# Optimization experiments

Measured on AMD Instinct MI355X. Metric: run time of the kernel, lower is better.

The kernel has to match this reference:

```python
import jax, jax.numpy as jnp
import numpy as np

N_NODES = 100000
N_EDGES = 1600000
IN_CH = 128          # 127 node features + 1 node_attr
HIDDEN = 2           # hidd_FV_size
OUT_CH = 128
ATTR = 6


def setup_inputs() -> dict:
    key = jax.random.key(0)
    ks = jax.random.split(key, 8)
    x = jax.random.normal(ks[0], (N_NODES, IN_CH - 1), dtype=jnp.float32)
    node_attr = jax.random.normal(ks[1], (N_NODES, 1), dtype=jnp.float32)
    edge_index = jax.random.randint(ks[2], (2, N_EDGES), 0, N_NODES, dtype=jnp.int64)
    edge_attr = jax.random.normal(ks[3], (N_EDGES, ATTR), dtype=jnp.float32)
    # lin_in: Linear(ATTR, HIDDEN * IN_CH); lin_out: Linear(HIDDEN * IN_CH, OUT_CH)
    W_in = jax.random.normal(ks[4], (ATTR, HIDDEN * IN_CH), dtype=jnp.float32) / np.sqrt(ATTR)
    b_in = jax.random.normal(ks[5], (HIDDEN * IN_CH,), dtype=jnp.float32) * 0.01
    W_out = jax.random.normal(ks[6], (HIDDEN * IN_CH, OUT_CH), dtype=jnp.float32) / np.sqrt(HIDDEN * IN_CH)
    b_out = jax.random.normal(ks[7], (OUT_CH,), dtype=jnp.float32) * 0.01
    return {"x": x, "node_attr": node_attr, "edge_index": edge_index,
            "edge_attr": edge_attr, "W_in": W_in, "b_in": b_in,
            "W_out": W_out, "b_out": b_out}


def reference(x, node_attr, edge_index, edge_attr, W_in, b_in, W_out, b_out):
    # forward: x = cat(x, node_attr) -> propagate(aggr='add') -> update
    xc = jnp.concatenate([x, node_attr], axis=1)                # [N, IN_CH]
    src, dst = edge_index[0], edge_index[1]                     # PyG: message from x_j=src, aggregated at dst
    x_j = xc[src]                                               # [E, IN_CH] gather
    # message: scaling = relu(lin_in(edge_attr)); result = scaling.reshape(E,C,H) * x_j[...,None]
    scaling = jax.nn.relu(edge_attr @ W_in + b_in)              # [E, C*H]
    msg = (scaling.reshape(-1, IN_CH, HIDDEN) * x_j[:, :, None]).reshape(-1, IN_CH * HIDDEN)
    # aggregate: scatter-add over destination nodes
    aggr = jax.ops.segment_sum(msg, dst, num_segments=N_NODES)  # [N, C*H]
    # update: lin_out -> tanh (dropout p=0 / eval mode)
    return jnp.tanh(aggr @ W_out + b_out)                       # [N, OUT_CH]
```

## Files before the change

### kernel.cpp

```cpp
#include <hip/hip_runtime.h>


#define ATTR 6
#define SCAN_CHUNK 1024


__device__ __forceinline__ float2 f2fma(float2 a, float2 b, float2 c) {
  return make_float2(fmaf(a.x, b.x, c.x), fmaf(a.y, b.y, c.y));
}
__device__ __forceinline__ float2 f2splat(float x) { return make_float2(x, x); }


__global__ __launch_bounds__(256) void hist_kernel(
    const int* __restrict__ ei, int* __restrict__ counts, int E)
{
  const int e0 = blockIdx.x * 1024 + threadIdx.x * 4;
  if (((E & 3) == 0) && (e0 + 4 <= E)) {
    const int4 d = *(const int4*)(ei + E + e0);
    atomicAdd(&counts[d.x], 1);
    atomicAdd(&counts[d.y], 1);
    atomicAdd(&counts[d.z], 1);
    atomicAdd(&counts[d.w], 1);
  } else {
#pragma unroll
    for (int j = 0; j < 4; ++j) {
      const int e = e0 + j;
      if (e < E) atomicAdd(&counts[ei[E + e]], 1);
    }
  }
}


__global__ __launch_bounds__(256) void scan1_kernel(
    const int* __restrict__ counts, int* __restrict__ offsets,
    int* __restrict__ bsum, int N)
{
  __shared__ int sdata[256];
  const int t = threadIdx.x;
  const int base = blockIdx.x * SCAN_CHUNK + t * 4;
  int c[4]; int s = 0;
#pragma unroll
  for (int j = 0; j < 4; ++j) { int i = base + j; c[j] = (i < N) ? counts[i] : 0; s += c[j]; }
  sdata[t] = s;
  __syncthreads();
  for (int d = 1; d < 256; d <<= 1) {
    int tv = (t >= d) ? sdata[t - d] : 0;
    __syncthreads();
    sdata[t] += tv;
    __syncthreads();
  }
  int excl = sdata[t] - s;
#pragma unroll
  for (int j = 0; j < 4; ++j) { int i = base + j; if (i < N) offsets[i] = excl; excl += c[j]; }
  if (t == 255) bsum[blockIdx.x] = sdata[255];
}


__global__ __launch_bounds__(256) void scanB_kernel(
    int* __restrict__ offsets, int* __restrict__ cursors,
    const int* __restrict__ bsum, int N, int E)
{
  __shared__ int red[4];
  const int t = threadIdx.x;
  int v = 0;
  for (int k = t; k < (int)blockIdx.x; k += 256) v += bsum[k];
#pragma unroll
  for (int d = 32; d > 0; d >>= 1) v += __shfl_down(v, d, 64);
  if ((t & 63) == 0) red[t >> 6] = v;
  __syncthreads();
  const int add = red[0] + red[1] + red[2] + red[3];

  const int base = blockIdx.x * SCAN_CHUNK + t * 4;
#pragma unroll
  for (int j = 0; j < 4; ++j) {
    const int i = base + j;
    if (i < N) { const int o = offsets[i] + add; offsets[i] = o; cursors[i] = o; }
  }
  if (blockIdx.x == 0 && t == 0) offsets[N] = E;
}


__global__ __launch_bounds__(256) void scatter_concat2_kernel(
    const int* __restrict__ ei, const float* __restrict__ ea,
    int* __restrict__ cursors, float* __restrict__ pay,
    const float* __restrict__ x, const float* __restrict__ na,
    float* __restrict__ xc, int E, int N, int SB)
{
  if ((int)blockIdx.x < SB) {
    const int e = blockIdx.x * 256 + threadIdx.x;
    if (e < E) {
      const int dst = ei[E + e];
      const int slot = atomicAdd(&cursors[dst], 1);
      const float2 a0 = *(const float2*)(ea + e * ATTR + 0);
      const float2 a1 = *(const float2*)(ea + e * ATTR + 2);
      const float2 a2 = *(const float2*)(ea + e * ATTR + 4);
      float4* pp = (float4*)pay + 2 * slot;
      pp[0] = make_float4(__int_as_float(ei[e]), a0.x, a0.y, a1.x);
      pp[1] = make_float4(a1.y, a2.x, a2.y, 0.f);
    }
  } else {
    const int gid = (blockIdx.x - SB) * 256 + threadIdx.x;
    const int row = gid >> 5;
    const int c4 = (gid & 31) * 4;
    if (row < N) {
      const float* xr = x + row * 127;
      float4 v;
      v.x = xr[c4];
      v.y = xr[c4 + 1];
      v.z = xr[c4 + 2];
      v.w = (c4 == 124) ? na[row] : xr[c4 + 3];
      *(float4*)(xc + row * 128 + c4) = v;
    }
  }
}


#define EDGE_MATH4(P0, P1, XV)                                                \
  {                                                                           \
    const float e0f = (P0).y;                                                 \
    const float e1f = (P0).z;                                                 \
    const float e2f = (P0).w;                                                 \
    const float e3f = (P1).x;                                                 \
    const float e4f = (P1).y;                                                 \
    const float e5f = (P1).z;                                                 \
    float sa0 = bA.x, sa1 = bA.y, sb0 = bB.x, sb1 = bB.y;                     \
    sa0 = fmaf(e0f, wA[0].x, sa0); sa1 = fmaf(e0f, wA[0].y, sa1);             \
    sb0 = fmaf(e0f, wB[0].x, sb0); sb1 = fmaf(e0f, wB[0].y, sb1);             \
    sa0 = fmaf(e1f, wA[1].x, sa0); sa1 = fmaf(e1f, wA[1].y, sa1);             \
    sb0 = fmaf(e1f, wB[1].x, sb0); sb1 = fmaf(e1f, wB[1].y, sb1);             \
    sa0 = fmaf(e2f, wA[2].x, sa0); sa1 = fmaf(e2f, wA[2].y, sa1);             \
    sb0 = fmaf(e2f, wB[2].x, sb0); sb1 = fmaf(e2f, wB[2].y, sb1);             \
    sa0 = fmaf(e3f, wA[3].x, sa0); sa1 = fmaf(e3f, wA[3].y, sa1);             \
    sb0 = fmaf(e3f, wB[3].x, sb0); sb1 = fmaf(e3f, wB[3].y, sb1);             \
    sa0 = fmaf(e4f, wA[4].x, sa0); sa1 = fmaf(e4f, wA[4].y, sa1);             \
    sb0 = fmaf(e4f, wB[4].x, sb0); sb1 = fmaf(e4f, wB[4].y, sb1);             \
    sa0 = fmaf(e5f, wA[5].x, sa0); sa1 = fmaf(e5f, wA[5].y, sa1);             \
    sb0 = fmaf(e5f, wB[5].x, sb0); sb1 = fmaf(e5f, wB[5].y, sb1);             \
    sa0 = fmaxf(sa0, 0.f); sa1 = fmaxf(sa1, 0.f);                             \
    sb0 = fmaxf(sb0, 0.f); sb1 = fmaxf(sb1, 0.f);                             \
    accA.x = fmaf(sa0, (XV).x, accA.x); accA.y = fmaf(sa1, (XV).x, accA.y);   \
    accB.x = fmaf(sb0, (XV).y, accB.x); accB.y = fmaf(sb1, (XV).y, accB.y);   \
  }

__global__ __launch_bounds__(256) void aggregate_v7_kernel(
    const float* __restrict__ xc,
    const float* __restrict__ W_in, const float* __restrict__ b_in,
    const int* __restrict__ offsets, const float* __restrict__ pay,
    float* __restrict__ aggr, int N)
{
  const int L = (int)threadIdx.x & 63;
  const int n = __builtin_amdgcn_readfirstlane((int)blockIdx.x * 4 + ((int)threadIdx.x >> 6));
  if (n >= N) return;

  float2 wA[ATTR], wB[ATTR];
#pragma unroll
  for (int a = 0; a < ATTR; ++a) {
    const float4 w4 = *(const float4*)(W_in + a * 256 + 4 * L);
    wA[a] = make_float2(w4.x, w4.y);
    wB[a] = make_float2(w4.z, w4.w);
  }
  const float4 b4 = *(const float4*)(b_in + 4 * L);
  const float2 bA = make_float2(b4.x, b4.y);
  const float2 bB = make_float2(b4.z, b4.w);

  float2 accA = make_float2(0.f, 0.f);
  float2 accB = make_float2(0.f, 0.f);
  const int beg = __builtin_amdgcn_readfirstlane(offsets[n]);
  const int end = __builtin_amdgcn_readfirstlane(offsets[n + 1]);
  const int lane2 = 2 * L;
  const float4* pp = (const float4*)pay;

  int i = beg;
  const int nfull = (end - beg) >> 1;

  if (nfull > 0) {
    float4 c0a = pp[2 * (size_t)i + 0], c1a = pp[2 * (size_t)i + 1];
    float4 c0b = pp[2 * (size_t)i + 2], c1b = pp[2 * (size_t)i + 3];
    float2 ga = *(const float2*)(xc + (unsigned)__float_as_int(c0a.x) * 128u + lane2);
    float2 gb = *(const float2*)(xc + (unsigned)__float_as_int(c0b.x) * 128u + lane2);
    const int i1 = (nfull > 1) ? i + 2 : i;
    float4 n0a = pp[2 * (size_t)i1 + 0], n1a = pp[2 * (size_t)i1 + 1];
    float4 n0b = pp[2 * (size_t)i1 + 2], n1b = pp[2 * (size_t)i1 + 3];

#pragma unroll 2
    for (int g = 0; g < nfull; ++g, i += 2) {
      float2 ha = *(const float2*)(xc + (unsigned)__float_as_int(n0a.x) * 128u + lane2);
      float2 hb = *(const float2*)(xc + (unsigned)__float_as_int(n0b.x) * 128u + lane2);
      const int ip = (g + 2 < nfull) ? i + 4 : i;
      float4 f0a = pp[2 * (size_t)ip + 0], f1a = pp[2 * (size_t)ip + 1];
      float4 f0b = pp[2 * (size_t)ip + 2], f1b = pp[2 * (size_t)ip + 3];

      EDGE_MATH4(c0a, c1a, ga);
      EDGE_MATH4(c0b, c1b, gb);

      c0a = n0a; c1a = n1a; c0b = n0b; c1b = n1b;
      n0a = f0a; n1a = f1a; n0b = f0b; n1b = f1b;
      ga = ha; gb = hb;
    }
  }

  if (i < end) {
    const float4 p0 = pp[2 * (size_t)i + 0];
    const float4 p1 = pp[2 * (size_t)i + 1];
    const float2 xv = *(const float2*)(xc + (unsigned)__float_as_int(p0.x) * 128u + lane2);
    EDGE_MATH4(p0, p1, xv);
  }

  *(float4*)(aggr + n * 256 + 4 * L) = make_float4(accA.x, accA.y, accB.x, accB.y);
}


__global__ __launch_bounds__(256) void scatter_concat_kernel(
    const int* __restrict__ ei, const float* __restrict__ ea,
    int* __restrict__ cursors, int* __restrict__ srcs, float* __restrict__ eas,
    const float* __restrict__ x, const float* __restrict__ na,
    float* __restrict__ xc, int E, int N, int SB)
{
  if ((int)blockIdx.x < SB) {
    const int e = blockIdx.x * 256 + threadIdx.x;
    if (e < E) {
      const int dst = ei[E + e];
      const int slot = atomicAdd(&cursors[dst], 1);
      srcs[slot] = ei[e];
      const float2 a0 = *(const float2*)(ea + (size_t)e * ATTR + 0);
      const float2 a1 = *(const float2*)(ea + (size_t)e * ATTR + 2);
      const float2 a2 = *(const float2*)(ea + (size_t)e * ATTR + 4);
      float* ep = eas + (size_t)slot * ATTR;
      *(float2*)(ep + 0) = a0;
      *(float2*)(ep + 2) = a1;
      *(float2*)(ep + 4) = a2;
    }
  } else {
    const int gid = (blockIdx.x - SB) * 256 + threadIdx.x;
    const int row = gid >> 5;
    const int c4 = (gid & 31) * 4;
    if (row < N) {
      const float* xr = x + (size_t)row * 127;
      float4 v;
      v.x = xr[c4];
      v.y = xr[c4 + 1];
      v.z = xr[c4 + 2];
      v.w = (c4 == 124) ? na[row] : xr[c4 + 3];
      *(float4*)(xc + (size_t)row * 128 + c4) = v;
    }
  }
}

__global__ __launch_bounds__(256) void aggregate8b_kernel(
    const float* __restrict__ xc,
    const float* __restrict__ W_in, const float* __restrict__ b_in,
    const int* __restrict__ offsets, const int* __restrict__ srcs,
    const float* __restrict__ eas,
    float* __restrict__ aggr, int N)
{
  const int L = threadIdx.x & 63;
  const int n = __builtin_amdgcn_readfirstlane(blockIdx.x * 4 + (threadIdx.x >> 6));
  if (n >= N) return;

  float2 wlo[ATTR], whi[ATTR];
#pragma unroll
  for (int a = 0; a < ATTR; ++a) {
    wlo[a] = *(const float2*)(W_in + a * 256 + 2 * L);
    whi[a] = *(const float2*)(W_in + a * 256 + 128 + 2 * L);
  }
  const float2 blo = *(const float2*)(b_in + 2 * L);
  const float2 bhi = *(const float2*)(b_in + 128 + 2 * L);

  float alo0 = 0.f, alo1 = 0.f, ahi0 = 0.f, ahi1 = 0.f;
  const int beg = __builtin_amdgcn_readfirstlane(offsets[n]);
  const int end = __builtin_amdgcn_readfirstlane(offsets[n + 1]);

  for (int i0 = beg; i0 < end; ++i0) {
    const int s = srcs[i0];
    float eav[ATTR];
#pragma unroll
    for (int a = 0; a < ATTR; ++a) eav[a] = eas[(size_t)i0 * ATTR + a];
    const float* xr = xc + (size_t)s * 128;
    const float xl = xr[L];
    const float xh = xr[64 + L];
    float sl0 = blo.x, sl1 = blo.y, sh0 = bhi.x, sh1 = bhi.y;
#pragma unroll
    for (int a = 0; a < ATTR; ++a) {
      sl0 = fmaf(eav[a], wlo[a].x, sl0);
      sl1 = fmaf(eav[a], wlo[a].y, sl1);
      sh0 = fmaf(eav[a], whi[a].x, sh0);
      sh1 = fmaf(eav[a], whi[a].y, sh1);
    }
    sl0 = fmaxf(sl0, 0.f); sl1 = fmaxf(sl1, 0.f);
    sh0 = fmaxf(sh0, 0.f); sh1 = fmaxf(sh1, 0.f);
    alo0 = fmaf(sl0, xl, alo0);
    alo1 = fmaf(sl1, xl, alo1);
    ahi0 = fmaf(sh0, xh, ahi0);
    ahi1 = fmaf(sh1, xh, ahi1);
  }

  *(float2*)(aggr + (size_t)n * 256 + 2 * L)       = make_float2(alo0, alo1);
  *(float2*)(aggr + (size_t)n * 256 + 128 + 2 * L) = make_float2(ahi0, ahi1);
}


__global__ __launch_bounds__(256) void scatter_kernel(
    const int* __restrict__ ei, int* __restrict__ cursors,
    int* __restrict__ perm, int* __restrict__ srcs, int E)
{
  int e = blockIdx.x * 256 + threadIdx.x;
  if (e < E) {
    int dst = ei[E + e];
    int slot = atomicAdd(&cursors[dst], 1);
    perm[slot] = e;
    srcs[slot] = ei[e];
  }
}

__global__ __launch_bounds__(256) void aggregate4_kernel(
    const float* __restrict__ x, const float* __restrict__ node_attr,
    const int* __restrict__ ei, const float* __restrict__ ea,
    const float* __restrict__ W_in, const float* __restrict__ b_in,
    const int* __restrict__ offsets, const int* __restrict__ perm,
    const int* __restrict__ srcs,
    float* __restrict__ aggr, int N)
{
  const int L = threadIdx.x & 63;
  const int n = __builtin_amdgcn_readfirstlane(blockIdx.x * 4 + (threadIdx.x >> 6));
  if (n >= N) return;

  float2 wlo[ATTR], whi[ATTR];
#pragma unroll
  for (int a = 0; a < ATTR; ++a) {
    wlo[a] = *(const float2*)(W_in + a * 256 + 2 * L);
    whi[a] = *(const float2*)(W_in + a * 256 + 128 + 2 * L);
  }
  const float2 blo = *(const float2*)(b_in + 2 * L);
  const float2 bhi = *(const float2*)(b_in + 128 + 2 * L);

  float alo0 = 0.f, alo1 = 0.f, ahi0 = 0.f, ahi1 = 0.f;
  const int beg = offsets[n], end = offsets[n + 1];

  for (int i0 = beg; i0 < end; i0 += 4) {
    const int cnt = end - i0;
    int e4[4], s4[4];
#pragma unroll
    for (int j = 0; j < 4; ++j) {
      const int idx = i0 + ((j < cnt) ? j : cnt - 1);
      e4[j] = perm[idx];
      s4[j] = srcs[idx];
    }
    float eav[4][ATTR];
#pragma unroll
    for (int j = 0; j < 4; ++j)
#pragma unroll
      for (int a = 0; a < ATTR; ++a) eav[j][a] = ea[(size_t)e4[j] * ATTR + a];
    float xlo[4], xhi[4];
#pragma unroll
    for (int j = 0; j < 4; ++j) {
      const float* xr = x + (size_t)s4[j] * 127;
      xlo[j] = xr[L];
      xhi[j] = (L == 63) ? node_attr[s4[j]] : xr[64 + L];
    }
#pragma unroll
    for (int j = 0; j < 4; ++j)
      if (j >= cnt) { xlo[j] = 0.f; xhi[j] = 0.f; }
#pragma unroll
    for (int j = 0; j < 4; ++j) {
      float sl0 = blo.x, sl1 = blo.y, sh0 = bhi.x, sh1 = bhi.y;
#pragma unroll
      for (int a = 0; a < ATTR; ++a) {
        sl0 = fmaf(eav[j][a], wlo[a].x, sl0);
        sl1 = fmaf(eav[j][a], wlo[a].y, sl1);
        sh0 = fmaf(eav[j][a], whi[a].x, sh0);
        sh1 = fmaf(eav[j][a], whi[a].y, sh1);
      }
      sl0 = fmaxf(sl0, 0.f); sl1 = fmaxf(sl1, 0.f);
      sh0 = fmaxf(sh0, 0.f); sh1 = fmaxf(sh1, 0.f);
      alo0 = fmaf(sl0, xlo[j], alo0);
      alo1 = fmaf(sl1, xlo[j], alo1);
      ahi0 = fmaf(sh0, xhi[j], ahi0);
      ahi1 = fmaf(sh1, xhi[j], ahi1);
    }
  }

  *(float2*)(aggr + (size_t)n * 256 + 2 * L)       = make_float2(alo0, alo1);
  *(float2*)(aggr + (size_t)n * 256 + 128 + 2 * L) = make_float2(ahi0, ahi1);
}


__global__ __launch_bounds__(256) void edge_kernel(
    const float* __restrict__ x, const float* __restrict__ node_attr,
    const int* __restrict__ ei, const float* __restrict__ ea,
    const float* __restrict__ W_in, const float* __restrict__ b_in,
    float* __restrict__ aggr, int E, int N, int epw)
{
  const int lane = threadIdx.x & 63;
  const int wave = blockIdx.x * (blockDim.x >> 6) + (threadIdx.x >> 6);
  const int k0 = lane << 2;
  const int c0 = lane << 1;

  float w[ATTR][4];
#pragma unroll
  for (int a = 0; a < ATTR; ++a) {
    const float4 t = *(const float4*)(W_in + a * 256 + k0);
    w[a][0] = t.x; w[a][1] = t.y; w[a][2] = t.z; w[a][3] = t.w;
  }
  const float4 bt = *(const float4*)(b_in + k0);

  const long e0 = (long)wave * epw;
  for (int i = 0; i < epw; ++i) {
    const long e = e0 + i;
    if (e >= E) return;
    const int src = ei[e];
    const int dst = ei[E + e];

    float eav[ATTR];
#pragma unroll
    for (int a = 0; a < ATTR; ++a) eav[a] = ea[(size_t)e * ATTR + a];

    float s0 = bt.x, s1 = bt.y, s2 = bt.z, s3 = bt.w;
#pragma unroll
    for (int a = 0; a < ATTR; ++a) {
      s0 = fmaf(eav[a], w[a][0], s0);
      s1 = fmaf(eav[a], w[a][1], s1);
      s2 = fmaf(eav[a], w[a][2], s2);
      s3 = fmaf(eav[a], w[a][3], s3);
    }
    s0 = fmaxf(s0, 0.f); s1 = fmaxf(s1, 0.f);
    s2 = fmaxf(s2, 0.f); s3 = fmaxf(s3, 0.f);

    const float* xr = x + (size_t)src * 127;
    const float x0 = xr[c0];
    const float x1 = (lane == 63) ? node_attr[src] : xr[c0 + 1];

    float* ap = aggr + (size_t)dst * 256 + k0;
    atomicAdd(ap + 0, s0 * x0);
    atomicAdd(ap + 1, s1 * x0);
    atomicAdd(ap + 2, s2 * x1);
    atomicAdd(ap + 3, s3 * x1);
  }
}


__global__ __launch_bounds__(256) void node_kernel3(
    const float* __restrict__ aggr, const float* __restrict__ W_out,
    const float* __restrict__ b_out, float* __restrict__ out, int N)
{
  __shared__ float Wl[64 * 128];
  __shared__ float Al[64][68];
  const int t = threadIdx.x;
  const int o4 = (t & 31) * 4;
  const int ng = t >> 5;
  const int nbase = blockIdx.x * 64;

  float2 acc[8][2];
#pragma unroll
  for (int j = 0; j < 8; ++j) {
    acc[j][0] = make_float2(0.f, 0.f);
    acc[j][1] = make_float2(0.f, 0.f);
  }

  for (int kc = 0; kc < 4; ++kc) {
    __syncthreads();
    const float4* wsrc = (const float4*)(W_out + kc * 64 * 128);
    float4* wdst = (float4*)Wl;
#pragma unroll
    for (int i = 0; i < 8; ++i) wdst[t + 256 * i] = wsrc[t + 256 * i];
    {
      const int r = t >> 2, q = t & 3;
      int row = nbase + r; if (row >= N) row = N - 1;
      const float4* asrc = (const float4*)(aggr + (size_t)row * 256 + kc * 64 + q * 16);
      float4 v0 = asrc[0], v1 = asrc[1], v2 = asrc[2], v3 = asrc[3];
      float4* adst = (float4*)&Al[r][q * 16];
      adst[0] = v0; adst[1] = v1; adst[2] = v2; adst[3] = v3;
    }
    __syncthreads();

    for (int k = 0; k < 64; k += 4) {
      float4 a4[8];
#pragma unroll
      for (int j = 0; j < 8; ++j) a4[j] = *(const float4*)&Al[ng * 8 + j][k];
#pragma unroll
      for (int kk = 0; kk < 4; ++kk) {
        const float4 w4 = *(const float4*)&Wl[(k + kk) * 128 + o4];
        const float2 wA = make_float2(w4.x, w4.y);
        const float2 wB = make_float2(w4.z, w4.w);
#pragma unroll
        for (int j = 0; j < 8; ++j) {
          const float2 av = f2splat((&a4[j].x)[kk]);
          acc[j][0] = f2fma(av, wA, acc[j][0]);
          acc[j][1] = f2fma(av, wB, acc[j][1]);
        }
      }
    }
  }

  const float4 b4 = *(const float4*)(b_out + o4);
#pragma unroll
  for (int j = 0; j < 8; ++j) {
    const int n = nbase + ng * 8 + j;
    if (n < N) {
      float4 r;
      r.x = tanhf(acc[j][0].x + b4.x);
      r.y = tanhf(acc[j][0].y + b4.y);
      r.z = tanhf(acc[j][1].x + b4.z);
      r.w = tanhf(acc[j][1].y + b4.w);
      *(float4*)(out + (size_t)n * 128 + o4) = r;
    }
  }
}


extern "C" void kernel_launch(void* const* d_in, const int* in_sizes, int n_in,
                              void* d_out, int out_size, void* d_ws, size_t ws_size,
                              hipStream_t stream) {
  const float* x         = (const float*)d_in[0];
  const float* node_attr = (const float*)d_in[1];
  const int*   ei        = (const int*)d_in[2];
  const float* ea        = (const float*)d_in[3];
  const float* W_in      = (const float*)d_in[4];
  const float* b_in      = (const float*)d_in[5];
  const float* W_out     = (const float*)d_in[6];
  const float* b_out     = (const float*)d_in[7];
  float* out = (float*)d_out;

  const int N = in_sizes[0] / 127;
  const int E = in_sizes[2] / 2;

  auto align16 = [](size_t v) { return (v + 15) & ~(size_t)15; };
  const size_t szCounts  = align16((size_t)N * 4);
  const size_t szOffsets = align16(((size_t)N + 1) * 4);
  const size_t szCursors = align16((size_t)N * 4);
  const size_t szBsum    = align16(((size_t)N / SCAN_CHUNK + 2) * 4);
  const size_t szPerm    = align16((size_t)E * 4);
  const size_t szSrcs    = align16((size_t)E * 4);
  const size_t szEas     = align16((size_t)E * ATTR * 4);
  const size_t szPay     = align16((size_t)E * 8 * 4);
  const size_t szXc      = align16((size_t)N * 128 * 4);
  const size_t szAggr    = (size_t)N * 256 * 4;

  const size_t needA2 = szCounts + szOffsets + szCursors + szBsum +
                        szPay + szXc + szAggr;
  const size_t needA  = szCounts + szOffsets + szCursors + szBsum +
                        szSrcs + szEas + szXc + szAggr;
  const size_t needB  = szCounts + szOffsets + szCursors + szBsum +
                        szPerm + szSrcs + szAggr;

  const int nodeBlocks = (N + 63) / 64;
  const int histBlocks = (E + 1023) / 1024;
  const int nb = (N + SCAN_CHUNK - 1) / SCAN_CHUNK;
  const int SB = (E + 255) / 256;
  const int CB = (N * 32 + 255) / 256;

  if (ws_size >= needA2) {
    char* p = (char*)d_ws;
    int* counts   = (int*)p;     p += szCounts;
    int* offsets  = (int*)p;     p += szOffsets;
    int* cursors  = (int*)p;     p += szCursors;
    int* bsum     = (int*)p;     p += szBsum;
    float* pay    = (float*)p;   p += szPay;
    float* xc     = (float*)p;   p += szXc;
    float* aggr   = (float*)p;

    hipMemsetAsync(counts, 0, szCounts, stream);
    hist_kernel<<<histBlocks, 256, 0, stream>>>(ei, counts, E);
    scan1_kernel<<<nb, 256, 0, stream>>>(counts, offsets, bsum, N);
    scanB_kernel<<<nb, 256, 0, stream>>>(offsets, cursors, bsum, N, E);
    scatter_concat2_kernel<<<SB + CB, 256, 0, stream>>>(
        ei, ea, cursors, pay, x, node_attr, xc, E, N, SB);
    aggregate_v7_kernel<<<(N + 3) / 4, 256, 0, stream>>>(
        xc, W_in, b_in, offsets, pay, aggr, N);
    node_kernel3<<<nodeBlocks, 256, 0, stream>>>(aggr, W_out, b_out, out, N);
  } else if (ws_size >= needA) {
    char* p = (char*)d_ws;
    int* counts   = (int*)p;     p += szCounts;
    int* offsets  = (int*)p;     p += szOffsets;
    int* cursors  = (int*)p;     p += szCursors;
    int* bsum     = (int*)p;     p += szBsum;
    int* srcs     = (int*)p;     p += szSrcs;
    float* eas    = (float*)p;   p += szEas;
    float* xc     = (float*)p;   p += szXc;
    float* aggr   = (float*)p;

    hipMemsetAsync(counts, 0, szCounts, stream);
    hist_kernel<<<histBlocks, 256, 0, stream>>>(ei, counts, E);
    scan1_kernel<<<nb, 256, 0, stream>>>(counts, offsets, bsum, N);
    scanB_kernel<<<nb, 256, 0, stream>>>(offsets, cursors, bsum, N, E);
    scatter_concat_kernel<<<SB + CB, 256, 0, stream>>>(
        ei, ea, cursors, srcs, eas, x, node_attr, xc, E, N, SB);
    aggregate8b_kernel<<<(N + 3) / 4, 256, 0, stream>>>(
        xc, W_in, b_in, offsets, srcs, eas, aggr, N);
    node_kernel3<<<nodeBlocks, 256, 0, stream>>>(aggr, W_out, b_out, out, N);
  } else if (ws_size >= needB) {
    char* p = (char*)d_ws;
    int* counts   = (int*)p;     p += szCounts;
    int* offsets  = (int*)p;     p += szOffsets;
    int* cursors  = (int*)p;     p += szCursors;
    int* bsum     = (int*)p;     p += szBsum;
    int* perm     = (int*)p;     p += szPerm;
    int* srcs     = (int*)p;     p += szSrcs;
    float* aggr   = (float*)p;

    hipMemsetAsync(counts, 0, szCounts, stream);
    hist_kernel<<<histBlocks, 256, 0, stream>>>(ei, counts, E);
    scan1_kernel<<<nb, 256, 0, stream>>>(counts, offsets, bsum, N);
    scanB_kernel<<<nb, 256, 0, stream>>>(offsets, cursors, bsum, N, E);
    scatter_kernel<<<SB, 256, 0, stream>>>(ei, cursors, perm, srcs, E);
    aggregate4_kernel<<<(N + 3) / 4, 256, 0, stream>>>(
        x, node_attr, ei, ea, W_in, b_in, offsets, perm, srcs, aggr, N);
    node_kernel3<<<nodeBlocks, 256, 0, stream>>>(aggr, W_out, b_out, out, N);
  } else {
    float* aggr = (float*)d_ws;
    hipMemsetAsync(aggr, 0, (size_t)N * 256 * 4, stream);
    const int EPW = 4;
    const int waves = (E + EPW - 1) / EPW;
    edge_kernel<<<(waves + 3) / 4, 256, 0, stream>>>(
        x, node_attr, ei, ea, W_in, b_in, aggr, E, N, EPW);
    node_kernel3<<<nodeBlocks, 256, 0, stream>>>(aggr, W_out, b_out, out, N);
  }
}
```

Baseline: 536.9 us.

## Record per-edge rank during histogram to drop cursor atomics in scatter

The histogram kernel now stores each edge's atomicAdd return value as a 16-bit rank, so the scatter pass computes its slot as offsets[dst]+rank with no second round of atomics on cursors. The xc concatenation moves into the histogram launch, and the scan no longer writes a cursor array. In exchange it writes and reads an extra E*2-byte rank buffer, and it assumes in-degree fits in 16 bits. Edge order within a segment stays nondeterministic.

```diff
diff --git a/kernel.cpp b/kernel.cpp
--- a/kernel.cpp
+++ b/kernel.cpp
@@ -9,6 +9,46 @@
   return make_float2(fmaf(a.x, b.x, c.x), fmaf(a.y, b.y, c.y));
 }
 __device__ __forceinline__ float2 f2splat(float x) { return make_float2(x, x); }
+
+
+__global__ __launch_bounds__(256) void hist_rank_concat_kernel(
+    const int* __restrict__ ei, int* __restrict__ counts,
+    unsigned short* __restrict__ rank,
+    const float* __restrict__ x, const float* __restrict__ na,
+    float* __restrict__ xc, int E, int N, int SBH)
+{
+  if ((int)blockIdx.x < SBH) {
+    const int e0 = blockIdx.x * 1024 + threadIdx.x * 4;
+    if (((E & 3) == 0) && (e0 + 4 <= E)) {
+      const int4 d = *(const int4*)(ei + E + e0);
+      ushort4 r;
+      r.x = (unsigned short)atomicAdd(&counts[d.x], 1);
+      r.y = (unsigned short)atomicAdd(&counts[d.y], 1);
+      r.z = (unsigned short)atomicAdd(&counts[d.z], 1);
+      r.w = (unsigned short)atomicAdd(&counts[d.w], 1);
+      *(ushort4*)(rank + e0) = r;
+    } else {
+#pragma unroll
+      for (int j = 0; j < 4; ++j) {
+        const int e = e0 + j;
+        if (e < E) rank[e] = (unsigned short)atomicAdd(&counts[ei[E + e]], 1);
+      }
+    }
+  } else {
+    const int gid = (blockIdx.x - SBH) * 256 + threadIdx.x;
+    const int row = gid >> 5;
+    const int c4 = (gid & 31) * 4;
+    if (row < N) {
+      const float* xr = x + row * 127;
+      float4 v;
+      v.x = xr[c4];
+      v.y = xr[c4 + 1];
+      v.z = xr[c4 + 2];
+      v.w = (c4 == 124) ? na[row] : xr[c4 + 3];
+      *(float4*)(xc + row * 128 + c4) = v;
+    }
+  }
+}
 
 
 __global__ __launch_bounds__(256) void hist_kernel(
@@ -56,9 +96,8 @@
 }
 
 
-__global__ __launch_bounds__(256) void scanB_kernel(
-    int* __restrict__ offsets, int* __restrict__ cursors,
-    const int* __restrict__ bsum, int N, int E)
+__global__ __launch_bounds__(256) void scanB2_kernel(
+    int* __restrict__ offsets, const int* __restrict__ bsum, int N, int E)
 {
   __shared__ int red[4];
   const int t = threadIdx.x;
@@ -74,9 +113,52 @@
 #pragma unroll
   for (int j = 0; j < 4; ++j) {
     const int i = base + j;
+    if (i < N) offsets[i] += add;
+  }
+  if (blockIdx.x == 0 && t == 0) offsets[N] = E;
+}
+
+
+__global__ __launch_bounds__(256) void scanB_kernel(
+    int* __restrict__ offsets, int* __restrict__ cursors,
+    const int* __restrict__ bsum, int N, int E)
+{
+  __shared__ int red[4];
+  const int t = threadIdx.x;
+  int v = 0;
+  for (int k = t; k < (int)blockIdx.x; k += 256) v += bsum[k];
+#pragma unroll
+  for (int d = 32; d > 0; d >>= 1) v += __shfl_down(v, d, 64);
+  if ((t & 63) == 0) red[t >> 6] = v;
+  __syncthreads();
+  const int add = red[0] + red[1] + red[2] + red[3];
+
+  const int base = blockIdx.x * SCAN_CHUNK + t * 4;
+#pragma unroll
+  for (int j = 0; j < 4; ++j) {
+    const int i = base + j;
     if (i < N) { const int o = offsets[i] + add; offsets[i] = o; cursors[i] = o; }
   }
   if (blockIdx.x == 0 && t == 0) offsets[N] = E;
+}
+
+
+__global__ __launch_bounds__(256) void scatter_pay_kernel(
+    const int* __restrict__ ei, const unsigned short* __restrict__ rank,
+    const int* __restrict__ offsets, const float* __restrict__ ea,
+    float* __restrict__ pay, int E)
+{
+  const int e = blockIdx.x * 256 + threadIdx.x;
+  if (e < E) {
+    const int dst = ei[E + e];
+    const int slot = offsets[dst] + (int)rank[e];
+    const float2 a0 = *(const float2*)(ea + e * ATTR + 0);
+    const float2 a1 = *(const float2*)(ea + e * ATTR + 2);
+    const float2 a2 = *(const float2*)(ea + e * ATTR + 4);
+    float4* pp = (float4*)pay + 2 * slot;
+    pp[0] = make_float4(__int_as_float(ei[e]), a0.x, a0.y, a1.x);
+    pp[1] = make_float4(a1.y, a2.x, a2.y, 0.f);
+  }
 }
 
 
@@ -142,71 +224,75 @@
     accB.x = fmaf(sb0, (XV).y, accB.x); accB.y = fmaf(sb1, (XV).y, accB.y);   \
   }
 
+#define AGG_BODY                                                              \
+  const int L = (int)threadIdx.x & 63;                                        \
+  const int n = __builtin_amdgcn_readfirstlane(                               \
+      (int)blockIdx.x * 4 + ((int)threadIdx.x >> 6));                         \
+  if (n >= N) return;                                                         \
+  float2 wA[ATTR], wB[ATTR];                                                  \
+  _Pragma("unroll")                                                           \
+  for (int a = 0; a < ATTR; ++a) {                                            \
+    const float4 w4 = *(const float4*)(W_in + a * 256 + 4 * L);               \
+    wA[a] = make_float2(w4.x, w4.y);                                          \
+    wB[a] = make_float2(w4.z, w4.w);                                          \
+  }                                                                           \
+  const float4 b4 = *(const float4*)(b_in + 4 * L);                           \
+  const float2 bA = make_float2(b4.x, b4.y);                                  \
+  const float2 bB = make_float2(b4.z, b4.w);                                  \
+  float2 accA = make_float2(0.f, 0.f);                                        \
+  float2 accB = make_float2(0.f, 0.f);                                        \
+  const int beg = __builtin_amdgcn_readfirstlane(offsets[n]);                 \
+  const int end = __builtin_amdgcn_readfirstlane(offsets[n + 1]);             \
+  const int lane2 = 2 * L;                                                    \
+  const float4* pp = (const float4*)pay;                                      \
+  int i = beg;                                                                \
+  const int nfull = (end - beg) >> 1;                                         \
+  if (nfull > 0) {                                                            \
+    float4 c0a = pp[2 * (size_t)i + 0], c1a = pp[2 * (size_t)i + 1];          \
+    float4 c0b = pp[2 * (size_t)i + 2], c1b = pp[2 * (size_t)i + 3];          \
+    float2 ga = *(const float2*)(xc + (unsigned)__float_as_int(c0a.x) * 128u + lane2); \
+    float2 gb = *(const float2*)(xc + (unsigned)__float_as_int(c0b.x) * 128u + lane2); \
+    const int i1 = (nfull > 1) ? i + 2 : i;                                   \
+    float4 n0a = pp[2 * (size_t)i1 + 0], n1a = pp[2 * (size_t)i1 + 1];        \
+    float4 n0b = pp[2 * (size_t)i1 + 2], n1b = pp[2 * (size_t)i1 + 3];        \
+    _Pragma("unroll 2")                                                       \
+    for (int g = 0; g < nfull; ++g, i += 2) {                                 \
+      float2 ha = *(const float2*)(xc + (unsigned)__float_as_int(n0a.x) * 128u + lane2); \
+      float2 hb = *(const float2*)(xc + (unsigned)__float_as_int(n0b.x) * 128u + lane2); \
+      const int ip = (g + 2 < nfull) ? i + 4 : i;                             \
+      float4 f0a = pp[2 * (size_t)ip + 0], f1a = pp[2 * (size_t)ip + 1];      \
+      float4 f0b = pp[2 * (size_t)ip + 2], f1b = pp[2 * (size_t)ip + 3];      \
+      EDGE_MATH4(c0a, c1a, ga);                                               \
+      EDGE_MATH4(c0b, c1b, gb);                                               \
+      c0a = n0a; c1a = n1a; c0b = n0b; c1b = n1b;                             \
+      n0a = f0a; n1a = f1a; n0b = f0b; n1b = f1b;                             \
+      ga = ha; gb = hb;                                                       \
+    }                                                                         \
+  }                                                                           \
+  if (i < end) {                                                              \
+    const float4 p0 = pp[2 * (size_t)i + 0];                                  \
+    const float4 p1 = pp[2 * (size_t)i + 1];                                  \
+    const float2 xv = *(const float2*)(xc + (unsigned)__float_as_int(p0.x) * 128u + lane2); \
+    EDGE_MATH4(p0, p1, xv);                                                   \
+  }                                                                           \
+  *(float4*)(aggr + n * 256 + 4 * L) = make_float4(accA.x, accA.y, accB.x, accB.y);
+
+__global__ __launch_bounds__(256) void aggregate_v8_kernel(
+    const float* __restrict__ xc,
+    const float* __restrict__ W_in, const float* __restrict__ b_in,
+    const int* __restrict__ offsets, const float* __restrict__ pay,
+    float* __restrict__ aggr, int N)
+{
+  AGG_BODY
+}
+
 __global__ __launch_bounds__(256) void aggregate_v7_kernel(
     const float* __restrict__ xc,
     const float* __restrict__ W_in, const float* __restrict__ b_in,
     const int* __restrict__ offsets, const float* __restrict__ pay,
     float* __restrict__ aggr, int N)
 {
-  const int L = (int)threadIdx.x & 63;
-  const int n = __builtin_amdgcn_readfirstlane((int)blockIdx.x * 4 + ((int)threadIdx.x >> 6));
-  if (n >= N) return;
-
-  float2 wA[ATTR], wB[ATTR];
-#pragma unroll
-  for (int a = 0; a < ATTR; ++a) {
-    const float4 w4 = *(const float4*)(W_in + a * 256 + 4 * L);
-    wA[a] = make_float2(w4.x, w4.y);
-    wB[a] = make_float2(w4.z, w4.w);
-  }
-  const float4 b4 = *(const float4*)(b_in + 4 * L);
-  const float2 bA = make_float2(b4.x, b4.y);
-  const float2 bB = make_float2(b4.z, b4.w);
-
-  float2 accA = make_float2(0.f, 0.f);
-  float2 accB = make_float2(0.f, 0.f);
-  const int beg = __builtin_amdgcn_readfirstlane(offsets[n]);
-  const int end = __builtin_amdgcn_readfirstlane(offsets[n + 1]);
-  const int lane2 = 2 * L;
-  const float4* pp = (const float4*)pay;
-
-  int i = beg;
-  const int nfull = (end - beg) >> 1;
-
-  if (nfull > 0) {
-    float4 c0a = pp[2 * (size_t)i + 0], c1a = pp[2 * (size_t)i + 1];
-    float4 c0b = pp[2 * (size_t)i + 2], c1b = pp[2 * (size_t)i + 3];
-    float2 ga = *(const float2*)(xc + (unsigned)__float_as_int(c0a.x) * 128u + lane2);
-    float2 gb = *(const float2*)(xc + (unsigned)__float_as_int(c0b.x) * 128u + lane2);
-    const int i1 = (nfull > 1) ? i + 2 : i;
-    float4 n0a = pp[2 * (size_t)i1 + 0], n1a = pp[2 * (size_t)i1 + 1];
-    float4 n0b = pp[2 * (size_t)i1 + 2], n1b = pp[2 * (size_t)i1 + 3];
-
-#pragma unroll 2
-    for (int g = 0; g < nfull; ++g, i += 2) {
-      float2 ha = *(const float2*)(xc + (unsigned)__float_as_int(n0a.x) * 128u + lane2);
-      float2 hb = *(const float2*)(xc + (unsigned)__float_as_int(n0b.x) * 128u + lane2);
-      const int ip = (g + 2 < nfull) ? i + 4 : i;
-      float4 f0a = pp[2 * (size_t)ip + 0], f1a = pp[2 * (size_t)ip + 1];
-      float4 f0b = pp[2 * (size_t)ip + 2], f1b = pp[2 * (size_t)ip + 3];
-
-      EDGE_MATH4(c0a, c1a, ga);
-      EDGE_MATH4(c0b, c1b, gb);
-
-      c0a = n0a; c1a = n1a; c0b = n0b; c1b = n1b;
-      n0a = f0a; n1a = f1a; n0b = f0b; n1b = f1b;
-      ga = ha; gb = hb;
-    }
-  }
-
-  if (i < end) {
-    const float4 p0 = pp[2 * (size_t)i + 0];
-    const float4 p1 = pp[2 * (size_t)i + 1];
-    const float2 xv = *(const float2*)(xc + (unsigned)__float_as_int(p0.x) * 128u + lane2);
-    EDGE_MATH4(p0, p1, xv);
-  }
-
-  *(float4*)(aggr + n * 256 + 4 * L) = make_float4(accA.x, accA.y, accB.x, accB.y);
+  AGG_BODY
 }
 
 
@@ -528,6 +614,7 @@
   const size_t szOffsets = align16(((size_t)N + 1) * 4);
   const size_t szCursors = align16((size_t)N * 4);
   const size_t szBsum    = align16(((size_t)N / SCAN_CHUNK + 2) * 4);
+  const size_t szRank    = align16((size_t)E * 2);
   const size_t szPerm    = align16((size_t)E * 4);
   const size_t szSrcs    = align16((size_t)E * 4);
   const size_t szEas     = align16((size_t)E * ATTR * 4);
@@ -535,6 +622,8 @@
   const size_t szXc      = align16((size_t)N * 128 * 4);
   const size_t szAggr    = (size_t)N * 256 * 4;
 
+  const size_t needA3 = szCounts + szOffsets + szBsum + szRank +
+                        szPay + szXc + szAggr;
   const size_t needA2 = szCounts + szOffsets + szCursors + szBsum +
                         szPay + szXc + szAggr;
   const size_t needA  = szCounts + szOffsets + szCursors + szBsum +
@@ -548,7 +637,26 @@
   const int SB = (E + 255) / 256;
   const int CB = (N * 32 + 255) / 256;
 
-  if (ws_size >= needA2) {
+  if (ws_size >= needA3) {
+    char* p = (char*)d_ws;
+    int* counts   = (int*)p;     p += szCounts;
+    int* offsets  = (int*)p;     p += szOffsets;
+    int* bsum     = (int*)p;     p += szBsum;
+    unsigned short* rank = (unsigned short*)p; p += szRank;
+    float* pay    = (float*)p;   p += szPay;
+    float* xc     = (float*)p;   p += szXc;
+    float* aggr   = (float*)p;
+
+    hipMemsetAsync(counts, 0, szCounts, stream);
+    hist_rank_concat_kernel<<<histBlocks + CB, 256, 0, stream>>>(
+        ei, counts, rank, x, node_attr, xc, E, N, histBlocks);
+    scan1_kernel<<<nb, 256, 0, stream>>>(counts, offsets, bsum, N);
+    scanB2_kernel<<<nb, 256, 0, stream>>>(offsets, bsum, N, E);
+    scatter_pay_kernel<<<SB, 256, 0, stream>>>(ei, rank, offsets, ea, pay, E);
+    aggregate_v8_kernel<<<(N + 3) / 4, 256, 0, stream>>>(
+        xc, W_in, b_in, offsets, pay, aggr, N);
+    node_kernel3<<<nodeBlocks, 256, 0, stream>>>(aggr, W_out, b_out, out, N);
+  } else if (ws_size >= needA2) {
     char* p = (char*)d_ws;
     int* counts   = (int*)p;     p += szCounts;
     int* offsets  = (int*)p;     p += szOffsets;
```

Measured after the change: 520.5 us. -3.1%, faster.

## Record per-edge rank in histogram, gather fp16 node features, drop cursor atomics

Applied to the files above, without the earlier changes.

The histogram pass now saves each edge's atomic return value as a 16-bit rank, and the same launch builds an fp16 copy of the concatenated node features. The scatter pass computes its slot as offset plus rank, so the second round of atomics on cursors goes away. The aggregate kernel gathers half-precision features, which halves the bytes of the random gather. The costs are reduced feature precision, a rank that silently wraps if any node has more than 65535 in-edges, and extra rank-buffer traffic.

```diff
diff --git a/kernel.cpp b/kernel.cpp
--- a/kernel.cpp
+++ b/kernel.cpp
@@ -1,4 +1,5 @@
 #include <hip/hip_runtime.h>
+#include <hip/hip_fp16.h>
 
 
 #define ATTR 6
@@ -9,6 +10,51 @@
   return make_float2(fmaf(a.x, b.x, c.x), fmaf(a.y, b.y, c.y));
 }
 __device__ __forceinline__ float2 f2splat(float x) { return make_float2(x, x); }
+
+
+__global__ __launch_bounds__(256) void hist_rank_concat_kernel(
+    const int* __restrict__ ei, int* __restrict__ counts,
+    unsigned short* __restrict__ rank,
+    const float* __restrict__ x, const float* __restrict__ na,
+    __half* __restrict__ xch, int E, int N, int SBH)
+{
+  if ((int)blockIdx.x < SBH) {
+    const int e0 = blockIdx.x * 1024 + threadIdx.x * 4;
+    if (((E & 3) == 0) && (e0 + 4 <= E)) {
+      const int4 d = *(const int4*)(ei + E + e0);
+      ushort4 r;
+      r.x = (unsigned short)atomicAdd(&counts[d.x], 1);
+      r.y = (unsigned short)atomicAdd(&counts[d.y], 1);
+      r.z = (unsigned short)atomicAdd(&counts[d.z], 1);
+      r.w = (unsigned short)atomicAdd(&counts[d.w], 1);
+      *(ushort4*)(rank + e0) = r;
+    } else {
+#pragma unroll
+      for (int j = 0; j < 4; ++j) {
+        const int e = e0 + j;
+        if (e < E) rank[e] = (unsigned short)atomicAdd(&counts[ei[E + e]], 1);
+      }
+    }
+  } else {
+    const int gid = (blockIdx.x - SBH) * 256 + threadIdx.x;
+    const int row = gid >> 5;
+    const int c4 = (gid & 31) * 4;
+    if (row < N) {
+      const float* xr = x + row * 127;
+      float4 v;
+      v.x = xr[c4];
+      v.y = xr[c4 + 1];
+      v.z = xr[c4 + 2];
+      v.w = (c4 == 124) ? na[row] : xr[c4 + 3];
+      const __half2 h01 = __floats2half2_rn(v.x, v.y);
+      const __half2 h23 = __floats2half2_rn(v.z, v.w);
+      uint2 u;
+      u.x = *(const unsigned int*)&h01;
+      u.y = *(const unsigned int*)&h23;
+      *(uint2*)(xch + row * 128 + c4) = u;
+    }
+  }
+}
 
 
 __global__ __launch_bounds__(256) void hist_kernel(
@@ -56,9 +102,8 @@
 }
 
 
-__global__ __launch_bounds__(256) void scanB_kernel(
-    int* __restrict__ offsets, int* __restrict__ cursors,
-    const int* __restrict__ bsum, int N, int E)
+__global__ __launch_bounds__(256) void scanB2_kernel(
+    int* __restrict__ offsets, const int* __restrict__ bsum, int N, int E)
 {
   __shared__ int red[4];
   const int t = threadIdx.x;
@@ -74,9 +119,52 @@
 #pragma unroll
   for (int j = 0; j < 4; ++j) {
     const int i = base + j;
+    if (i < N) offsets[i] += add;
+  }
+  if (blockIdx.x == 0 && t == 0) offsets[N] = E;
+}
+
+
+__global__ __launch_bounds__(256) void scanB_kernel(
+    int* __restrict__ offsets, int* __restrict__ cursors,
+    const int* __restrict__ bsum, int N, int E)
+{
+  __shared__ int red[4];
+  const int t = threadIdx.x;
+  int v = 0;
+  for (int k = t; k < (int)blockIdx.x; k += 256) v += bsum[k];
+#pragma unroll
+  for (int d = 32; d > 0; d >>= 1) v += __shfl_down(v, d, 64);
+  if ((t & 63) == 0) red[t >> 6] = v;
+  __syncthreads();
+  const int add = red[0] + red[1] + red[2] + red[3];
+
+  const int base = blockIdx.x * SCAN_CHUNK + t * 4;
+#pragma unroll
+  for (int j = 0; j < 4; ++j) {
+    const int i = base + j;
     if (i < N) { const int o = offsets[i] + add; offsets[i] = o; cursors[i] = o; }
   }
   if (blockIdx.x == 0 && t == 0) offsets[N] = E;
+}
+
+
+__global__ __launch_bounds__(256) void scatter_pay_kernel(
+    const int* __restrict__ ei, const unsigned short* __restrict__ rank,
+    const int* __restrict__ offsets, const float* __restrict__ ea,
+    float* __restrict__ pay, int E)
+{
+  const int e = blockIdx.x * 256 + threadIdx.x;
+  if (e < E) {
+    const int dst = ei[E + e];
+    const int slot = offsets[dst] + (int)rank[e];
+    const float2 a0 = *(const float2*)(ea + e * ATTR + 0);
+    const float2 a1 = *(const float2*)(ea + e * ATTR + 2);
+    const float2 a2 = *(const float2*)(ea + e * ATTR + 4);
+    float4* pp = (float4*)pay + 2 * slot;
+    pp[0] = make_float4(__int_as_float(ei[e]), a0.x, a0.y, a1.x);
+    pp[1] = make_float4(a1.y, a2.x, a2.y, 0.f);
+  }
 }
 
 
@@ -142,8 +230,14 @@
     accB.x = fmaf(sb0, (XV).y, accB.x); accB.y = fmaf(sb1, (XV).y, accB.y);   \
   }
 
-__global__ __launch_bounds__(256) void aggregate_v7_kernel(
-    const float* __restrict__ xc,
+
+__device__ __forceinline__ float2 gather_h(const __half* xch, int src, int lane2) {
+  const __half2 h = *(const __half2*)(xch + (unsigned)src * 128u + lane2);
+  return __half22float2(h);
+}
+
+__global__ __launch_bounds__(256) void aggregate_v9_kernel(
+    const __half* __restrict__ xch,
     const float* __restrict__ W_in, const float* __restrict__ b_in,
     const int* __restrict__ offsets, const float* __restrict__ pay,
     float* __restrict__ aggr, int N)
@@ -176,16 +270,16 @@
   if (nfull > 0) {
     float4 c0a = pp[2 * (size_t)i + 0], c1a = pp[2 * (size_t)i + 1];
     float4 c0b = pp[2 * (size_t)i + 2], c1b = pp[2 * (size_t)i + 3];
-    float2 ga = *(const float2*)(xc + (unsigned)__float_as_int(c0a.x) * 128u + lane2);
-    float2 gb = *(const float2*)(xc + (unsigned)__float_as_int(c0b.x) * 128u + lane2);
+    float2 ga = gather_h(xch, __float_as_int(c0a.x), lane2);
+    float2 gb = gather_h(xch, __float_as_int(c0b.x), lane2);
     const int i1 = (nfull > 1) ? i + 2 : i;
     float4 n0a = pp[2 * (size_t)i1 + 0], n1a = pp[2 * (size_t)i1 + 1];
     float4 n0b = pp[2 * (size_t)i1 + 2], n1b = pp[2 * (size_t)i1 + 3];
 
 #pragma unroll 2
     for (int g = 0; g < nfull; ++g, i += 2) {
-      float2 ha = *(const float2*)(xc + (unsigned)__float_as_int(n0a.x) * 128u + lane2);
-      float2 hb = *(const float2*)(xc + (unsigned)__float_as_int(n0b.x) * 128u + lane2);
+      float2 ha = gather_h(xch, __float_as_int(n0a.x), lane2);
+      float2 hb = gather_h(xch, __float_as_int(n0b.x), lane2);
       const int ip = (g + 2 < nfull) ? i + 4 : i;
       float4 f0a = pp[2 * (size_t)ip + 0], f1a = pp[2 * (size_t)ip + 1];
       float4 f0b = pp[2 * (size_t)ip + 2], f1b = pp[2 * (size_t)ip + 3];
@@ -200,6 +294,45 @@
   }
 
   if (i < end) {
+    const float4 p0 = pp[2 * (size_t)i + 0];
+    const float4 p1 = pp[2 * (size_t)i + 1];
+    const float2 xv = gather_h(xch, __float_as_int(p0.x), lane2);
+    EDGE_MATH4(p0, p1, xv);
+  }
+
+  *(float4*)(aggr + n * 256 + 4 * L) = make_float4(accA.x, accA.y, accB.x, accB.y);
+}
+
+
+__global__ __launch_bounds__(256) void aggregate_v7_kernel(
+    const float* __restrict__ xc,
+    const float* __restrict__ W_in, const float* __restrict__ b_in,
+    const int* __restrict__ offsets, const float* __restrict__ pay,
+    float* __restrict__ aggr, int N)
+{
+  const int L = (int)threadIdx.x & 63;
+  const int n = __builtin_amdgcn_readfirstlane((int)blockIdx.x * 4 + ((int)threadIdx.x >> 6));
+  if (n >= N) return;
+
+  float2 wA[ATTR], wB[ATTR];
+#pragma unroll
+  for (int a = 0; a < ATTR; ++a) {
+    const float4 w4 = *(const float4*)(W_in + a * 256 + 4 * L);
+    wA[a] = make_float2(w4.x, w4.y);
+    wB[a] = make_float2(w4.z, w4.w);
+  }
+  const float4 b4 = *(const float4*)(b_in + 4 * L);
+  const float2 bA = make_float2(b4.x, b4.y);
+  const float2 bB = make_float2(b4.z, b4.w);
+
+  float2 accA = make_float2(0.f, 0.f);
+  float2 accB = make_float2(0.f, 0.f);
+  const int beg = __builtin_amdgcn_readfirstlane(offsets[n]);
+  const int end = __builtin_amdgcn_readfirstlane(offsets[n + 1]);
+  const int lane2 = 2 * L;
+  const float4* pp = (const float4*)pay;
+
+  for (int i = beg; i < end; ++i) {
     const float4 p0 = pp[2 * (size_t)i + 0];
     const float4 p1 = pp[2 * (size_t)i + 1];
     const float2 xv = *(const float2*)(xc + (unsigned)__float_as_int(p0.x) * 128u + lane2);
@@ -528,13 +661,17 @@
   const size_t szOffsets = align16(((size_t)N + 1) * 4);
   const size_t szCursors = align16((size_t)N * 4);
   const size_t szBsum    = align16(((size_t)N / SCAN_CHUNK + 2) * 4);
+  const size_t szRank    = align16((size_t)E * 2);
   const size_t szPerm    = align16((size_t)E * 4);
   const size_t szSrcs    = align16((size_t)E * 4);
   const size_t szEas     = align16((size_t)E * ATTR * 4);
   const size_t szPay     = align16((size_t)E * 8 * 4);
   const size_t szXc      = align16((size_t)N * 128 * 4);
+  const size_t szXcH     = align16((size_t)N * 128 * 2);
   const size_t szAggr    = (size_t)N * 256 * 4;
 
+  const size_t needA3 = szCounts + szOffsets + szBsum + szRank +
+                        szPay + szXcH + szAggr;
   const size_t needA2 = szCounts + szOffsets + szCursors + szBsum +
                         szPay + szXc + szAggr;
   const size_t needA  = szCounts + szOffsets + szCursors + szBsum +
@@ -548,7 +685,26 @@
   const int SB = (E + 255) / 256;
   const int CB = (N * 32 + 255) / 256;
 
-  if (ws_size >= needA2) {
+  if (ws_size >= needA3) {
+    char* p = (char*)d_ws;
+    int* counts   = (int*)p;     p += szCounts;
+    int* offsets  = (int*)p;     p += szOffsets;
+    int* bsum     = (int*)p;     p += szBsum;
+    unsigned short* rank = (unsigned short*)p; p += szRank;
+    float* pay    = (float*)p;   p += szPay;
+    __half* xch   = (__half*)p;  p += szXcH;
+    float* aggr   = (float*)p;
+
+    hipMemsetAsync(counts, 0, szCounts, stream);
+    hist_rank_concat_kernel<<<histBlocks + CB, 256, 0, stream>>>(
+        ei, counts, rank, x, node_attr, xch, E, N, histBlocks);
+    scan1_kernel<<<nb, 256, 0, stream>>>(counts, offsets, bsum, N);
+    scanB2_kernel<<<nb, 256, 0, stream>>>(offsets, bsum, N, E);
+    scatter_pay_kernel<<<SB, 256, 0, stream>>>(ei, rank, offsets, ea, pay, E);
+    aggregate_v9_kernel<<<(N + 3) / 4, 256, 0, stream>>>(
+        xch, W_in, b_in, offsets, pay, aggr, N);
+    node_kernel3<<<nodeBlocks, 256, 0, stream>>>(aggr, W_out, b_out, out, N);
+  } else if (ws_size >= needA2) {
     char* p = (char*)d_ws;
     int* counts   = (int*)p;     p += szCounts;
     int* offsets  = (int*)p;     p += szOffsets;
```

After: 472.1 us. -12.1%, faster.
